# Kernel optimization log

Hardware: AMD Instinct MI355X
Metric: run time of the kernel (lower is better)

Reference implementation:

```python
import jax, jax.numpy as jnp
import numpy as np

B, T = 128, 512
V, D = 50000, 128
LSTM_SIZE = 256
H = LSTM_SIZE // 2  # per-direction hidden = 128
K = 32              # num_tags


def setup_inputs() -> dict:
    key = jax.random.key(0)
    ks = jax.random.split(key, 16)
    s = 0.05
    inputs = jax.random.randint(ks[0], (B, T), 0, V, dtype=jnp.int32)
    tags = jax.random.randint(ks[1], (B, T), 0, K, dtype=jnp.int32)
    emb = (jax.random.normal(ks[2], (V, D)) * s).at[0].set(0.0)  # padding_idx=0
    # LSTM params, PyTorch gate order [i,f,g,o]; dim0 of stacks = [fwd, bwd]
    w_ih_l0 = jax.random.normal(ks[3], (2, 4 * H, D)) * s
    w_hh_l0 = jax.random.normal(ks[4], (2, 4 * H, H)) * s
    b_l0 = jax.random.normal(ks[5], (2, 4 * H)) * s  # b_ih + b_hh combined
    w_ih_l1 = jax.random.normal(ks[6], (2, 4 * H, 2 * H)) * s
    w_hh_l1 = jax.random.normal(ks[7], (2, 4 * H, H)) * s
    b_l1 = jax.random.normal(ks[8], (2, 4 * H)) * s
    W_out = jax.random.normal(ks[9], (K, 2 * H)) * s
    b_out = jax.random.normal(ks[10], (K,)) * s
    start_t = jax.random.normal(ks[11], (K,)) * s
    end_t = jax.random.normal(ks[12], (K,)) * s
    trans = jax.random.normal(ks[13], (K, K)) * s
    return {"inputs": inputs, "tags": tags, "emb": emb,
            "w_ih_l0": w_ih_l0, "w_hh_l0": w_hh_l0, "b_l0": b_l0,
            "w_ih_l1": w_ih_l1, "w_hh_l1": w_hh_l1, "b_l1": b_l1,
            "W_out": W_out, "b_out": b_out,
            "start_t": start_t, "end_t": end_t, "trans": trans}


def _lstm_dir(xT, Wih, Whh, b, reverse):
    # xT: [T,B,Din] time-major
    Bn = xT.shape[1]
    Hn = Whh.shape[1]

    def step(carry, xt):
        h, c = carry
        z = xt @ Wih.T + h @ Whh.T + b  # [B,4H]
        i, f, g, o = jnp.split(z, 4, axis=-1)
        c = jax.nn.sigmoid(f) * c + jax.nn.sigmoid(i) * jnp.tanh(g)
        h = jax.nn.sigmoid(o) * jnp.tanh(c)
        return (h, c), h

    init = (jnp.zeros((Bn, Hn), xT.dtype), jnp.zeros((Bn, Hn), xT.dtype))
    _, hs = jax.lax.scan(step, init, xT, reverse=reverse)
    return hs  # [T,B,H], in original time order


def _bilstm_layer(xT, w_ih, w_hh, b):
    hf = _lstm_dir(xT, w_ih[0], w_hh[0], b[0], False)
    hb = _lstm_dir(xT, w_ih[1], w_hh[1], b[1], True)
    return jnp.concatenate([hf, hb], axis=-1)  # [T,B,2H]


def _viterbi(emT, start_t, end_t, trans):
    # emT: [T,B,K] time-major emissions; returns [B,T] int32 best tags
    score0 = start_t[None, :] + emT[0]  # [B,K]

    def step(score, em_t):
        # cand[b,i,j] = score[b,i] + trans[i,j] + em_t[b,j]
        cand = score[:, :, None] + trans[None] + em_t[:, None, :]
        return jnp.max(cand, axis=1), jnp.argmax(cand, axis=1).astype(jnp.int32)

    score, hist = jax.lax.scan(step, score0, emT[1:])  # hist: [T-1,B,K]
    score = score + end_t[None, :]
    last = jnp.argmax(score, axis=-1).astype(jnp.int32)  # [B]

    def back(tag, hist_t):
        prev = jnp.take_along_axis(hist_t, tag[:, None], axis=1)[:, 0]
        return prev, prev

    _, prevs = jax.lax.scan(back, last, hist, reverse=True)  # [T-1,B]
    return jnp.concatenate([prevs, last[None]], axis=0).T  # [B,T]


def reference(inputs, tags, emb, w_ih_l0, w_hh_l0, b_l0,
              w_ih_l1, w_hh_l1, b_l1, W_out, b_out,
              start_t, end_t, trans):
    # Embedding lookup -> time-major
    x = emb[inputs]                      # [B,T,D]
    xT = jnp.transpose(x, (1, 0, 2))     # [T,B,D]
    h1 = _bilstm_layer(xT, w_ih_l0, w_hh_l0, b_l0)   # [T,B,2H] (dropout is eval no-op)
    h2 = _bilstm_layer(h1, w_ih_l1, w_hh_l1, b_l1)   # [T,B,2H]
    emT = h2 @ W_out.T + b_out           # [T,B,K]
    return _viterbi(emT, start_t, end_t, trans)      # [B,T] int32
```

## Files before the change

kernel.cpp:

```cpp
#include <hip/hip_runtime.h>
#include <cmath>

static constexpr int NB   = 128;
static constexpr int NT   = 512;
static constexpr int ND   = 128;
static constexpr int NH   = 128;
static constexpr int NG4  = 512;
static constexpr int NKT  = 32;
static constexpr int CHUNK = 128;
static constexpr int NCH  = NT / CHUNK;

__device__ __forceinline__ float sigf(float x) { return 1.0f / (1.0f + expf(-x)); }

template <int DIN>
__global__ __launch_bounds__(256) void proj_gemm16x8(
    const float* __restrict__ Wih,
    const float* __restrict__ bias,
    const float* __restrict__ xsrc,
    const int*   __restrict__ inputs,
    float*       __restrict__ zin,
    int c)
{
    constexpr int KT = DIN / 16;
    __shared__ __align__(16) float A[2][16][128];
    __shared__ __align__(16) float Bs[2][16][256];
    __shared__ const float* rowp[128];

    const int bid = blockIdx.x;
    const int d  = bid >> 8;
    const int b  = (bid >> 1) & 127;
    const int ct = bid & 1;
    const int tid = threadIdx.x;
    const int tx = tid & 31;
    const int ty = tid >> 5;
    const int a_r = tid & 127;
    const int a_k = tid >> 7;

    if (tid < 128) {
        const int s = tid;
        const int ttl = c * CHUNK + s;
        const int t = d ? (NT - 1 - ttl) : ttl;
        if constexpr (DIN == 128) {
            rowp[tid] = xsrc + (size_t)inputs[b * NT + t] * ND;
        } else {
            rowp[tid] = xsrc + ((size_t)(b * NT + t)) * 256;
        }
    }
    __syncthreads();

    const float* arow = rowp[a_r];
    const float* wrow = Wih + ((size_t)(d * NG4 + ct * 256 + tid)) * DIN;

    float acc[16][8];
#pragma unroll
    for (int i = 0; i < 16; ++i)
#pragma unroll
        for (int n = 0; n < 8; ++n) acc[i][n] = 0.0f;

    float4 pa0 = *(const float4*)(arow + a_k * 8);
    float4 pa1 = *(const float4*)(arow + a_k * 8 + 4);
    float4 pb0 = *(const float4*)(wrow + 0);
    float4 pb1 = *(const float4*)(wrow + 4);
    float4 pb2 = *(const float4*)(wrow + 8);
    float4 pb3 = *(const float4*)(wrow + 12);

    for (int kt = 0; kt < KT; ++kt) {
        const int buf = kt & 1;
        A[buf][a_k * 8 + 0][a_r] = pa0.x; A[buf][a_k * 8 + 1][a_r] = pa0.y;
        A[buf][a_k * 8 + 2][a_r] = pa0.z; A[buf][a_k * 8 + 3][a_r] = pa0.w;
        A[buf][a_k * 8 + 4][a_r] = pa1.x; A[buf][a_k * 8 + 5][a_r] = pa1.y;
        A[buf][a_k * 8 + 6][a_r] = pa1.z; A[buf][a_k * 8 + 7][a_r] = pa1.w;
        Bs[buf][ 0][tid] = pb0.x; Bs[buf][ 1][tid] = pb0.y;
        Bs[buf][ 2][tid] = pb0.z; Bs[buf][ 3][tid] = pb0.w;
        Bs[buf][ 4][tid] = pb1.x; Bs[buf][ 5][tid] = pb1.y;
        Bs[buf][ 6][tid] = pb1.z; Bs[buf][ 7][tid] = pb1.w;
        Bs[buf][ 8][tid] = pb2.x; Bs[buf][ 9][tid] = pb2.y;
        Bs[buf][10][tid] = pb2.z; Bs[buf][11][tid] = pb2.w;
        Bs[buf][12][tid] = pb3.x; Bs[buf][13][tid] = pb3.y;
        Bs[buf][14][tid] = pb3.z; Bs[buf][15][tid] = pb3.w;
        __syncthreads();

        if (kt + 1 < KT) {
            const int k0 = (kt + 1) * 16;
            pa0 = *(const float4*)(arow + k0 + a_k * 8);
            pa1 = *(const float4*)(arow + k0 + a_k * 8 + 4);
            pb0 = *(const float4*)(wrow + k0 + 0);
            pb1 = *(const float4*)(wrow + k0 + 4);
            pb2 = *(const float4*)(wrow + k0 + 8);
            pb3 = *(const float4*)(wrow + k0 + 12);
        }

#pragma unroll 2
        for (int k = 0; k < 16; ++k) {
            float4 a0 = *(const float4*)&A[buf][k][ty * 16];
            float4 a1 = *(const float4*)&A[buf][k][ty * 16 + 4];
            float4 a2 = *(const float4*)&A[buf][k][ty * 16 + 8];
            float4 a3 = *(const float4*)&A[buf][k][ty * 16 + 12];
            float4 b0 = *(const float4*)&Bs[buf][k][tx * 4];
            float4 b1 = *(const float4*)&Bs[buf][k][128 + tx * 4];
            const float ar[16] = {a0.x, a0.y, a0.z, a0.w, a1.x, a1.y, a1.z, a1.w,
                                  a2.x, a2.y, a2.z, a2.w, a3.x, a3.y, a3.z, a3.w};
            const float br[8]  = {b0.x, b0.y, b0.z, b0.w, b1.x, b1.y, b1.z, b1.w};
#pragma unroll
            for (int i = 0; i < 16; ++i)
#pragma unroll
                for (int n = 0; n < 8; ++n) acc[i][n] += ar[i] * br[n];
        }
    }

    float4 bb0 = *(const float4*)(bias + d * NG4 + ct * 256 + tx * 4);
    float4 bb1 = *(const float4*)(bias + d * NG4 + ct * 256 + 128 + tx * 4);
#pragma unroll
    for (int i = 0; i < 16; ++i) {
        const int s = ty * 16 + i;
        float* zp = zin + (((size_t)(d * NB + b) * CHUNK + s)) * NG4 + ct * 256;
        float4 o0, o1;
        o0.x = acc[i][0] + bb0.x; o0.y = acc[i][1] + bb0.y;
        o0.z = acc[i][2] + bb0.z; o0.w = acc[i][3] + bb0.w;
        o1.x = acc[i][4] + bb1.x; o1.y = acc[i][5] + bb1.y;
        o1.z = acc[i][6] + bb1.z; o1.w = acc[i][7] + bb1.w;
        *(float4*)(zp + tx * 4) = o0;
        *(float4*)(zp + 128 + tx * 4) = o1;
    }
}

__global__ __launch_bounds__(512) void lstm_rec512(
    const float* __restrict__ Whh,
    const float* __restrict__ zin,
    float*       __restrict__ hout,
    float*       __restrict__ state_h,
    float*       __restrict__ state_c,
    int c)
{
    __shared__ __align__(16) float h_lds[128];
    __shared__ float p_lds[512];

    const int bid = blockIdx.x;
    const int d = bid >> 7, b = bid & 127;
    const int j = threadIdx.x;

    float w[128];
    const float* wrow = Whh + ((size_t)(d * NG4 + j)) * NH;
#pragma unroll
    for (int kk = 0; kk < 128; kk += 4) {
        float4 t4 = *(const float4*)(wrow + kk);
        w[kk] = t4.x; w[kk + 1] = t4.y; w[kk + 2] = t4.z; w[kk + 3] = t4.w;
    }

    float c_reg = 0.0f;
    if (j < 128) {
        float h0 = 0.0f;
        if (c != 0) {
            h0    = state_h[(d * NB + b) * NH + j];
            c_reg = state_c[(d * NB + b) * NH + j];
        }
        h_lds[j] = h0;
    }
    __syncthreads();

    const float* zb = zin + ((size_t)(d * NB + b)) * CHUNK * NG4;

    for (int s = 0; s < CHUNK; ++s) {
        float z0 = 0.f, z1 = 0.f, z2 = 0.f, z3 = 0.f;
        if (j < 128) {
            const float* zr = zb + (size_t)s * NG4;
            z0 = zr[j]; z1 = zr[128 + j]; z2 = zr[256 + j]; z3 = zr[384 + j];
        }
        float acc = 0.0f;
#pragma unroll
        for (int kk = 0; kk < 128; kk += 4) {
            float4 hv = *(const float4*)&h_lds[kk];
            acc += w[kk] * hv.x + w[kk + 1] * hv.y + w[kk + 2] * hv.z + w[kk + 3] * hv.w;
        }
        p_lds[j] = acc;
        __syncthreads();

        if (j < 128) {
            const float zi = z0 + p_lds[j];
            const float zf = z1 + p_lds[128 + j];
            const float zg = z2 + p_lds[256 + j];
            const float zo = z3 + p_lds[384 + j];
            const float ig = sigf(zi), fg = sigf(zf), og = sigf(zo);
            c_reg = fg * c_reg + ig * tanhf(zg);
            const float hn = og * tanhf(c_reg);
            const int ttl = c * CHUNK + s;
            const int t   = d ? (NT - 1 - ttl) : ttl;
            h_lds[j] = hn;
            hout[((size_t)(b * NT + t)) * 256 + d * NH + j] = hn;
        }
        __syncthreads();
    }

    if (j < 128) {
        state_h[(d * NB + b) * NH + j] = h_lds[j];
        state_c[(d * NB + b) * NH + j] = c_reg;
    }
}

__global__ __launch_bounds__(256) void emis_kernel(
    const float* __restrict__ h2,
    const float* __restrict__ Wout,
    const float* __restrict__ bout,
    float*       __restrict__ em)
{
    __shared__ float wt[256 * 32];
    __shared__ __align__(16) float hrow[8][256];

    const int tid = threadIdx.x;
    const int k = tid & 31;
    const int rl = tid >> 5;

    for (int e = tid; e < 8192; e += 256) {
        const int kk = e >> 8, cc = e & 255;
        wt[cc * 32 + kk] = Wout[e];
    }
    const float bk = bout[k];
    __syncthreads();

    const size_t base = (size_t)blockIdx.x * 64;
    for (int rr = 0; rr < 8; ++rr) {
        const size_t r0 = base + rr * 8;
        for (int e = tid; e < 512; e += 256) {
            ((float4*)&hrow[0][0])[e] = ((const float4*)(h2 + r0 * 256))[e];
        }
        __syncthreads();
        float acc = bk;
#pragma unroll 8
        for (int cc = 0; cc < 256; cc += 4) {
            float4 hv = *(const float4*)&hrow[rl][cc];
            acc += hv.x * wt[cc * 32 + k] + hv.y * wt[(cc + 1) * 32 + k] +
                   hv.z * wt[(cc + 2) * 32 + k] + hv.w * wt[(cc + 3) * 32 + k];
        }
        em[(r0 + rl) * NKT + k] = acc;
        __syncthreads();
    }
}

__global__ __launch_bounds__(64) void viterbi_v3(
    const float* __restrict__ em,
    const float* __restrict__ start_t,
    const float* __restrict__ end_t,
    const float* __restrict__ trans,
    int*         __restrict__ out)
{
    __shared__ __align__(16) float score_s[32];
    __shared__ unsigned char hist[(NT - 1) * 32];

    const int b = blockIdx.x;
    const int lane = threadIdx.x;
    const int j = lane & 31;
    const int h = lane >> 5;

    float tr_reg[16];
#pragma unroll
    for (int ii = 0; ii < 16; ++ii) tr_reg[ii] = trans[(h * 16 + ii) * 32 + j];
    const float et = end_t[j];

    const float* embase = em + (size_t)b * NT * NKT;
    if (lane < 32) score_s[j] = start_t[j] + embase[j];
    __syncthreads();

    float em_c  = embase[NKT + j];
    float em_p1 = embase[2 * NKT + j];

    for (int t = 1; t < NT; ++t) {
        const float em_p2 = (t + 2 < NT) ? embase[(size_t)(t + 2) * NKT + j] : 0.0f;

        float4 s0 = *(const float4*)&score_s[h * 16];
        float4 s1 = *(const float4*)&score_s[h * 16 + 4];
        float4 s2 = *(const float4*)&score_s[h * 16 + 8];
        float4 s3 = *(const float4*)&score_s[h * 16 + 12];
        const float sc[16] = {s0.x, s0.y, s0.z, s0.w, s1.x, s1.y, s1.z, s1.w,
                              s2.x, s2.y, s2.z, s2.w, s3.x, s3.y, s3.z, s3.w};

        float v[16];
#pragma unroll
        for (int ii = 0; ii < 16; ++ii) {
            v[ii] = (sc[ii] + tr_reg[ii]) + em_c;
        }
        float l1v[8]; int l1i[8];
#pragma unroll
        for (int p = 0; p < 8; ++p) {
            const bool L = v[2 * p] >= v[2 * p + 1];
            l1v[p] = L ? v[2 * p] : v[2 * p + 1];
            l1i[p] = L ? 2 * p : 2 * p + 1;
        }
        float l2v[4]; int l2i[4];
#pragma unroll
        for (int p = 0; p < 4; ++p) {
            const bool L = l1v[2 * p] >= l1v[2 * p + 1];
            l2v[p] = L ? l1v[2 * p] : l1v[2 * p + 1];
            l2i[p] = L ? l1i[2 * p] : l1i[2 * p + 1];
        }
        float l3v[2]; int l3i[2];
#pragma unroll
        for (int p = 0; p < 2; ++p) {
            const bool L = l2v[2 * p] >= l2v[2 * p + 1];
            l3v[p] = L ? l2v[2 * p] : l2v[2 * p + 1];
            l3i[p] = L ? l2i[2 * p] : l2i[2 * p + 1];
        }
        const bool L4 = l3v[0] >= l3v[1];
        const float best = L4 ? l3v[0] : l3v[1];
        const int   bi   = h * 16 + (L4 ? l3i[0] : l3i[1]);

        const float ob  = __shfl(best, lane ^ 32);
        const int   obi = __shfl(bi,   lane ^ 32);
        const bool take_other = h ? (ob >= best) : (ob > best);
        const float ns = take_other ? ob : best;
        const int  arg = take_other ? obi : bi;

        if (h == 0) {
            hist[(t - 1) * 32 + j] = (unsigned char)arg;
            score_s[j] = ns;
        }
        __syncthreads();

        em_c  = em_p1;
        em_p1 = em_p2;
    }

    float fv = score_s[j] + et;
    int fi = j;
#pragma unroll
    for (int dlt = 1; dlt <= 16; dlt <<= 1) {
        const float vo = __shfl_xor(fv, dlt);
        const int   io = __shfl_xor(fi, dlt);
        if (vo > fv || (vo == fv && io < fi)) { fv = vo; fi = io; }
    }

    if (lane == 0) {
        int tag = fi;
        out[b * NT + (NT - 1)] = tag;
        for (int t = NT - 2; t >= 0; --t) {
            tag = hist[t * 32 + tag];
            out[b * NT + t] = tag;
        }
    }
}

extern "C" void kernel_launch(void* const* d_in, const int* in_sizes, int n_in,
                              void* d_out, int out_size, void* d_ws, size_t ws_size,
                              hipStream_t stream) {
    const int*   inputs  = (const int*)d_in[0];
    const float* emb     = (const float*)d_in[2];
    const float* w_ih_l0 = (const float*)d_in[3];
    const float* w_hh_l0 = (const float*)d_in[4];
    const float* b_l0    = (const float*)d_in[5];
    const float* w_ih_l1 = (const float*)d_in[6];
    const float* w_hh_l1 = (const float*)d_in[7];
    const float* b_l1    = (const float*)d_in[8];
    const float* W_out   = (const float*)d_in[9];
    const float* b_out   = (const float*)d_in[10];
    const float* start_t = (const float*)d_in[11];
    const float* end_t   = (const float*)d_in[12];
    const float* trans   = (const float*)d_in[13];
    int* out = (int*)d_out;

    float* ws  = (float*)d_ws;
    float* zin = ws;
    float* h1  = zin + (size_t)2 * NB * CHUNK * NG4;
    float* h2  = h1 + (size_t)NB * NT * 256;
    float* sth = h2 + (size_t)NB * NT * 256;
    float* stc = sth + (size_t)2 * NB * NH;
    float* em  = stc + (size_t)2 * NB * NH;

    for (int c = 0; c < NCH; ++c) {
        proj_gemm16x8<128><<<512, 256, 0, stream>>>(w_ih_l0, b_l0, emb, inputs, zin, c);
        lstm_rec512<<<256, 512, 0, stream>>>(w_hh_l0, zin, h1, sth, stc, c);
    }
    for (int c = 0; c < NCH; ++c) {
        proj_gemm16x8<256><<<512, 256, 0, stream>>>(w_ih_l1, b_l1, h1, nullptr, zin, c);
        lstm_rec512<<<256, 512, 0, stream>>>(w_hh_l1, zin, h2, sth, stc, c);
    }
    emis_kernel<<<(NB * NT) / 64, 256, 0, stream>>>(h2, W_out, b_out, em);
    viterbi_v3<<<NB, 64, 0, stream>>>(em, start_t, end_t, trans, out);
}
```

Measured before the change: 2.195 ms.

## Stage LSTM gate inputs and outputs in LDS and restructure Viterbi kernel

The recurrent LSTM kernel now loads 16 timesteps of precomputed gate inputs into LDS at once and buffers 16 steps of hidden outputs before writing them back together. This takes global loads and scattered stores off the serial per-step critical path, and the dot product is split into eight partial sums for more instruction-level parallelism. The Viterbi kernel now copies the whole emission row and the transition matrix into LDS and uses a simple sequential max loop in place of the tree reduction. The projection GEMM is wrapped into two non-template kernels. The exchange is much more LDS per block (about 40 KB in the LSTM kernel, over 70 KB in Viterbi), and the Viterbi loop gains an extra barrier per step. Tie-breaking in the argmax also changes slightly.

```diff
diff --git a/kernel.cpp b/kernel.cpp
--- a/kernel.cpp
+++ b/kernel.cpp
@@ -13,7 +13,7 @@
 __device__ __forceinline__ float sigf(float x) { return 1.0f / (1.0f + expf(-x)); }
 
 template <int DIN>
-__global__ __launch_bounds__(256) void proj_gemm16x8(
+__device__ __forceinline__ void proj_body(
     const float* __restrict__ Wih,
     const float* __restrict__ bias,
     const float* __restrict__ xsrc,
@@ -124,7 +124,19 @@
     }
 }
 
-__global__ __launch_bounds__(512) void lstm_rec512(
+__global__ __launch_bounds__(256) void proj_l0(
+    const float* __restrict__ Wih, const float* __restrict__ bias,
+    const float* __restrict__ xsrc, const int* __restrict__ inputs,
+    float* __restrict__ zin, int c)
+{ proj_body<128>(Wih, bias, xsrc, inputs, zin, c); }
+
+__global__ __launch_bounds__(256) void proj_l1(
+    const float* __restrict__ Wih, const float* __restrict__ bias,
+    const float* __restrict__ xsrc, const int* __restrict__ inputs,
+    float* __restrict__ zin, int c)
+{ proj_body<256>(Wih, bias, xsrc, inputs, zin, c); }
+
+__global__ __launch_bounds__(512) void lstm_rec16(
     const float* __restrict__ Whh,
     const float* __restrict__ zin,
     float*       __restrict__ hout,
@@ -134,6 +146,8 @@
 {
     __shared__ __align__(16) float h_lds[128];
     __shared__ float p_lds[512];
+    __shared__ __align__(16) float z_lds[16][512];
+    __shared__ float hh[16][128];
 
     const int bid = blockIdx.x;
     const int d = bid >> 7, b = bid & 127;
@@ -160,35 +174,56 @@
 
     const float* zb = zin + ((size_t)(d * NB + b)) * CHUNK * NG4;
 
-    for (int s = 0; s < CHUNK; ++s) {
-        float z0 = 0.f, z1 = 0.f, z2 = 0.f, z3 = 0.f;
-        if (j < 128) {
-            const float* zr = zb + (size_t)s * NG4;
-            z0 = zr[j]; z1 = zr[128 + j]; z2 = zr[256 + j]; z3 = zr[384 + j];
-        }
-        float acc = 0.0f;
-#pragma unroll
-        for (int kk = 0; kk < 128; kk += 4) {
-            float4 hv = *(const float4*)&h_lds[kk];
-            acc += w[kk] * hv.x + w[kk + 1] * hv.y + w[kk + 2] * hv.z + w[kk + 3] * hv.w;
-        }
-        p_lds[j] = acc;
-        __syncthreads();
-
-        if (j < 128) {
-            const float zi = z0 + p_lds[j];
-            const float zf = z1 + p_lds[128 + j];
-            const float zg = z2 + p_lds[256 + j];
-            const float zo = z3 + p_lds[384 + j];
-            const float ig = sigf(zi), fg = sigf(zf), og = sigf(zo);
-            c_reg = fg * c_reg + ig * tanhf(zg);
-            const float hn = og * tanhf(c_reg);
-            const int ttl = c * CHUNK + s;
-            const int t   = d ? (NT - 1 - ttl) : ttl;
-            h_lds[j] = hn;
-            hout[((size_t)(b * NT + t)) * 256 + d * NH + j] = hn;
-        }
-        __syncthreads();
+    for (int s0 = 0; s0 < CHUNK; s0 += 16) {
+        const float4* zsrc = (const float4*)(zb + (size_t)s0 * NG4);
+        float4* zdst = (float4*)&z_lds[0][0];
+#pragma unroll
+        for (int it = 0; it < 4; ++it) {
+            zdst[it * 512 + j] = zsrc[it * 512 + j];
+        }
+        __syncthreads();
+
+        for (int ss = 0; ss < 16; ++ss) {
+            float ap[8];
+#pragma unroll
+            for (int g = 0; g < 8; ++g) {
+                float4 x0 = *(const float4*)&h_lds[g * 16];
+                float4 x1 = *(const float4*)&h_lds[g * 16 + 4];
+                float4 x2 = *(const float4*)&h_lds[g * 16 + 8];
+                float4 x3 = *(const float4*)&h_lds[g * 16 + 12];
+                ap[g] = w[g*16+ 0]*x0.x + w[g*16+ 1]*x0.y + w[g*16+ 2]*x0.z + w[g*16+ 3]*x0.w
+                      + w[g*16+ 4]*x1.x + w[g*16+ 5]*x1.y + w[g*16+ 6]*x1.z + w[g*16+ 7]*x1.w
+                      + w[g*16+ 8]*x2.x + w[g*16+ 9]*x2.y + w[g*16+10]*x2.z + w[g*16+11]*x2.w
+                      + w[g*16+12]*x3.x + w[g*16+13]*x3.y + w[g*16+14]*x3.z + w[g*16+15]*x3.w;
+            }
+            const float acc = ((ap[0] + ap[1]) + (ap[2] + ap[3]))
+                            + ((ap[4] + ap[5]) + (ap[6] + ap[7]));
+            p_lds[j] = acc;
+            __syncthreads();
+
+            if (j < 128) {
+                const float* zr = &z_lds[ss][0];
+                const float zi = zr[j]       + p_lds[j];
+                const float zf = zr[128 + j] + p_lds[128 + j];
+                const float zg = zr[256 + j] + p_lds[256 + j];
+                const float zo = zr[384 + j] + p_lds[384 + j];
+                const float ig = sigf(zi), fg = sigf(zf), og = sigf(zo);
+                c_reg = fg * c_reg + ig * tanhf(zg);
+                const float hn = og * tanhf(c_reg);
+                h_lds[j] = hn;
+                hh[ss][j] = hn;
+            }
+            __syncthreads();
+        }
+
+#pragma unroll
+        for (int it = 0; it < 4; ++it) {
+            const int idx = it * 512 + j;
+            const int ss = idx >> 7, jj = idx & 127;
+            const int ttl = c * CHUNK + s0 + ss;
+            const int t = d ? (NT - 1 - ttl) : ttl;
+            hout[((size_t)(b * NT + t)) * 256 + d * NH + jj] = hh[ss][jj];
+        }
     }
 
     if (j < 128) {
@@ -236,100 +271,64 @@
     }
 }
 
-__global__ __launch_bounds__(64) void viterbi_v3(
+__global__ __launch_bounds__(64) void viterbi_k(
     const float* __restrict__ em,
     const float* __restrict__ start_t,
     const float* __restrict__ end_t,
     const float* __restrict__ trans,
     int*         __restrict__ out)
 {
-    __shared__ __align__(16) float score_s[32];
+    __shared__ float score[32];
+    __shared__ float tr[1024];
+    __shared__ float fsc[32];
+    __shared__ __align__(16) float em_s[NT * NKT];
     __shared__ unsigned char hist[(NT - 1) * 32];
 
     const int b = blockIdx.x;
     const int lane = threadIdx.x;
-    const int j = lane & 31;
-    const int h = lane >> 5;
-
-    float tr_reg[16];
-#pragma unroll
-    for (int ii = 0; ii < 16; ++ii) tr_reg[ii] = trans[(h * 16 + ii) * 32 + j];
-    const float et = end_t[j];
+    const int j = lane & 31, h = lane >> 5;
 
     const float* embase = em + (size_t)b * NT * NKT;
-    if (lane < 32) score_s[j] = start_t[j] + embase[j];
-    __syncthreads();
-
-    float em_c  = embase[NKT + j];
-    float em_p1 = embase[2 * NKT + j];
+#pragma unroll 8
+    for (int e = lane; e < NT * NKT / 4; e += 64) {
+        ((float4*)em_s)[e] = ((const float4*)embase)[e];
+    }
+    for (int e = lane; e < 1024; e += 64) tr[e] = trans[e];
+    if (lane < 32) score[j] = start_t[j] + embase[j];
+    __syncthreads();
 
     for (int t = 1; t < NT; ++t) {
-        const float em_p2 = (t + 2 < NT) ? embase[(size_t)(t + 2) * NKT + j] : 0.0f;
-
-        float4 s0 = *(const float4*)&score_s[h * 16];
-        float4 s1 = *(const float4*)&score_s[h * 16 + 4];
-        float4 s2 = *(const float4*)&score_s[h * 16 + 8];
-        float4 s3 = *(const float4*)&score_s[h * 16 + 12];
-        const float sc[16] = {s0.x, s0.y, s0.z, s0.w, s1.x, s1.y, s1.z, s1.w,
-                              s2.x, s2.y, s2.z, s2.w, s3.x, s3.y, s3.z, s3.w};
-
-        float v[16];
+        const float em_j = em_s[t * NKT + j];
+        float best = -1e30f;
+        int bi = 0;
 #pragma unroll
         for (int ii = 0; ii < 16; ++ii) {
-            v[ii] = (sc[ii] + tr_reg[ii]) + em_c;
-        }
-        float l1v[8]; int l1i[8];
-#pragma unroll
-        for (int p = 0; p < 8; ++p) {
-            const bool L = v[2 * p] >= v[2 * p + 1];
-            l1v[p] = L ? v[2 * p] : v[2 * p + 1];
-            l1i[p] = L ? 2 * p : 2 * p + 1;
-        }
-        float l2v[4]; int l2i[4];
-#pragma unroll
-        for (int p = 0; p < 4; ++p) {
-            const bool L = l1v[2 * p] >= l1v[2 * p + 1];
-            l2v[p] = L ? l1v[2 * p] : l1v[2 * p + 1];
-            l2i[p] = L ? l1i[2 * p] : l1i[2 * p + 1];
-        }
-        float l3v[2]; int l3i[2];
-#pragma unroll
-        for (int p = 0; p < 2; ++p) {
-            const bool L = l2v[2 * p] >= l2v[2 * p + 1];
-            l3v[p] = L ? l2v[2 * p] : l2v[2 * p + 1];
-            l3i[p] = L ? l2i[2 * p] : l2i[2 * p + 1];
-        }
-        const bool L4 = l3v[0] >= l3v[1];
-        const float best = L4 ? l3v[0] : l3v[1];
-        const int   bi   = h * 16 + (L4 ? l3i[0] : l3i[1]);
-
+            const int i = h * 16 + ii;
+            const float v = (score[i] + tr[i * 32 + j]) + em_j;
+            if (v > best) { best = v; bi = i; }
+        }
         const float ob  = __shfl(best, lane ^ 32);
         const int   obi = __shfl(bi,   lane ^ 32);
-        const bool take_other = h ? (ob >= best) : (ob > best);
-        const float ns = take_other ? ob : best;
-        const int  arg = take_other ? obi : bi;
-
+        __syncthreads();
         if (h == 0) {
+            float ns; int arg;
+            if (ob > best) { ns = ob; arg = obi; }
+            else           { ns = best; arg = bi; }
+            score[j] = ns;
             hist[(t - 1) * 32 + j] = (unsigned char)arg;
-            score_s[j] = ns;
-        }
-        __syncthreads();
-
-        em_c  = em_p1;
-        em_p1 = em_p2;
-    }
-
-    float fv = score_s[j] + et;
-    int fi = j;
-#pragma unroll
-    for (int dlt = 1; dlt <= 16; dlt <<= 1) {
-        const float vo = __shfl_xor(fv, dlt);
-        const int   io = __shfl_xor(fi, dlt);
-        if (vo > fv || (vo == fv && io < fi)) { fv = vo; fi = io; }
-    }
-
+        }
+        __syncthreads();
+    }
+
+    if (lane < 32) fsc[j] = score[j] + end_t[j];
+    __syncthreads();
     if (lane == 0) {
-        int tag = fi;
+        float best = -1e30f; int bi = 0;
+        for (int i = 0; i < 32; ++i) {
+            const float v = fsc[i];
+            if (v > best) { best = v; bi = i; }
+        }
+        int tag = bi;
         out[b * NT + (NT - 1)] = tag;
         for (int t = NT - 2; t >= 0; --t) {
             tag = hist[t * 32 + tag];
@@ -365,13 +364,13 @@
     float* em  = stc + (size_t)2 * NB * NH;
 
     for (int c = 0; c < NCH; ++c) {
-        proj_gemm16x8<128><<<512, 256, 0, stream>>>(w_ih_l0, b_l0, emb, inputs, zin, c);
-        lstm_rec512<<<256, 512, 0, stream>>>(w_hh_l0, zin, h1, sth, stc, c);
+        proj_l0<<<512, 256, 0, stream>>>(w_ih_l0, b_l0, emb, inputs, zin, c);
+        lstm_rec16<<<256, 512, 0, stream>>>(w_hh_l0, zin, h1, sth, stc, c);
     }
     for (int c = 0; c < NCH; ++c) {
-        proj_gemm16x8<256><<<512, 256, 0, stream>>>(w_ih_l1, b_l1, h1, nullptr, zin, c);
-        lstm_rec512<<<256, 512, 0, stream>>>(w_hh_l1, zin, h2, sth, stc, c);
+        proj_l1<<<512, 256, 0, stream>>>(w_ih_l1, b_l1, h1, nullptr, zin, c);
+        lstm_rec16<<<256, 512, 0, stream>>>(w_hh_l1, zin, h2, sth, stc, c);
     }
     emis_kernel<<<(NB * NT) / 64, 256, 0, stream>>>(h2, W_out, b_out, em);
-    viterbi_v3<<<NB, 64, 0, stream>>>(em, start_t, end_t, trans, out);
-}
+    viterbi_k<<<NB, 64, 0, stream>>>(em, start_t, end_t, trans, out);
+}
```

Measured after the change: 2.315 ms. 1.05x slower.
